# Kernel tuning notes

Measured on AMD Instinct MI355X. Metric: run time of the kernel, lower is better.

The kernel has to match this reference:

```python
import jax, jax.numpy as jnp
import numpy as np

B, T, D = 16, 4096, 1024
UNITS = 1024


def setup_inputs() -> dict:
    key = jax.random.key(0)
    ks = jax.random.split(key, 8)
    s_in = 1.0 / np.sqrt(D)
    s_u = 1.0 / np.sqrt(UNITS)
    return {
        "hidden_state": jax.random.normal(ks[0], (B, D), jnp.float32),
        "encoder_output": jax.random.normal(ks[1], (B, T, D), jnp.float32),
        "W1": jax.random.normal(ks[2], (D, UNITS), jnp.float32) * s_in,
        "b1": jnp.zeros((UNITS,), jnp.float32),
        "W2": jax.random.normal(ks[3], (D, UNITS), jnp.float32) * s_in,
        "b2": jnp.zeros((UNITS,), jnp.float32),
        "V": jax.random.normal(ks[4], (UNITS, 1), jnp.float32) * s_u,
        "bv": jnp.zeros((1,), jnp.float32),
    }


def reference(hidden_state, encoder_output, W1, b1, W2, b2, V, bv):
    # Bahdanau additive attention: score = V(tanh(W1(h) + W2(enc)))
    h_proj = hidden_state @ W1 + b1                      # [B, U]
    e_proj = jnp.einsum("btd,du->btu", encoder_output, W2) + b2  # [B, T, U]
    feat = jnp.tanh(h_proj[:, None, :] + e_proj)          # [B, T, U]
    score = feat @ V + bv                                 # [B, T, 1]
    attention_weights = jax.nn.softmax(score, axis=1)     # [B, T, 1]
    context_vector = jnp.sum(attention_weights * encoder_output, axis=1)  # [B, D]
    return context_vector, attention_weights
```

## Files before the change

kernel.cpp:

```cpp
#include <hip/hip_runtime.h>
#include <hip/hip_bf16.h>
#include <math.h>

#define B_ 16
#define T_ 4096
#define D_ 1024
#define U_ 1024
#define M_ (B_*T_)

typedef __attribute__((ext_vector_type(8))) short short8;
typedef __attribute__((ext_vector_type(4))) short short4v;
typedef __attribute__((ext_vector_type(4))) float float4v;

static __device__ __forceinline__ short f2bf(float f) {
    unsigned u = __builtin_bit_cast(unsigned, f);
    u += 0x7FFFu + ((u >> 16) & 1u);
    return (short)(u >> 16);
}
static __device__ __forceinline__ float bf2f(short s) {
    unsigned u = ((unsigned)(unsigned short)s) << 16;
    return __builtin_bit_cast(float, u);
}
static __device__ __forceinline__ float fast_tanh(float x) {
    float c = fminf(fmaxf(2.f * x, -30.f), 30.f);
    float t = __expf(c);
    return __fdividef(t - 1.f, t + 1.f);
}

#define GLLDS(GP, LP) __builtin_amdgcn_global_load_lds( \
    (const __attribute__((address_space(1))) void*)(GP), \
    (__attribute__((address_space(3))) void*)(LP), 16, 0, 0)

__global__ void hb_kernel(const float* __restrict__ h, const float* __restrict__ W1,
                          const float* __restrict__ b1, const float* __restrict__ b2,
                          float* __restrict__ hbp) {
    int x = blockIdx.x;
    int kc = x >> 6;
    int gid = (x & 63) * 256 + threadIdx.x;
    int b = gid >> 10, u = gid & 1023;
    const float* hr = h + b * D_ + kc * 256;
    const float* w = W1 + (size_t)(kc * 256) * U_ + u;
    float s0 = 0.f, s1 = 0.f, s2 = 0.f, s3 = 0.f;
    for (int k = 0; k < 256; k += 4) {
        s0 += hr[k+0] * w[(size_t)(k+0) * U_];
        s1 += hr[k+1] * w[(size_t)(k+1) * U_];
        s2 += hr[k+2] * w[(size_t)(k+2) * U_];
        s3 += hr[k+3] * w[(size_t)(k+3) * U_];
    }
    float s = ((s0 + s1) + (s2 + s3));
    if (kc == 0) s += b1[u] + b2[u];
    hbp[kc * 16384 + gid] = s;
}

__global__ void convert_enc(const float* __restrict__ enc, short* __restrict__ encbf) {
    size_t g = (size_t)blockIdx.x * 256 + threadIdx.x;
    const float4v* p = (const float4v*)(enc + g * 16);
    float4v f0 = p[0], f1 = p[1], f2 = p[2], f3 = p[3];
    short8 a, b;
    a[0]=f2bf(f0[0]); a[1]=f2bf(f0[1]); a[2]=f2bf(f0[2]); a[3]=f2bf(f0[3]);
    a[4]=f2bf(f1[0]); a[5]=f2bf(f1[1]); a[6]=f2bf(f1[2]); a[7]=f2bf(f1[3]);
    b[0]=f2bf(f2[0]); b[1]=f2bf(f2[1]); b[2]=f2bf(f2[2]); b[3]=f2bf(f2[3]);
    b[4]=f2bf(f3[0]); b[5]=f2bf(f3[1]); b[6]=f2bf(f3[2]); b[7]=f2bf(f3[3]);
    short8* q = (short8*)(encbf + g * 16);
    q[0] = a; q[1] = b;
}

__global__ void convert_w2t(const float* __restrict__ W2, short* __restrict__ W2T) {
    __shared__ short t[64][65];
    int k0 = (blockIdx.x >> 4) * 64, u0 = (blockIdx.x & 15) * 64;
    int tx = threadIdx.x & 63, ty = threadIdx.x >> 6;
    #pragma unroll
    for (int r = 0; r < 16; ++r) {
        int kk = ty * 16 + r;
        t[kk][tx] = f2bf(W2[(size_t)(k0 + kk) * U_ + u0 + tx]);
    }
    __syncthreads();
    #pragma unroll
    for (int r = 0; r < 16; ++r) {
        int uu = ty * 16 + r;
        W2T[(size_t)(u0 + uu) * D_ + k0 + tx] = t[tx][uu];
    }
}

__global__ __launch_bounds__(512, 2) void gemm_score_8ph(
    const short* __restrict__ Abf,
    const short* __restrict__ W2T,
    const float* __restrict__ hbp,
    const float* __restrict__ V,
    float* __restrict__ scorepart)
{
    __shared__ __align__(16) short lds[65536];

    const int tid = threadIdx.x;
    const int g = blockIdx.x;
    const int c = g & 7, q = g >> 3;
    const int ntile = q & 3;
    const int mtile = (q >> 2) * 8 + c;
    const int row0 = mtile * 256, n0 = ntile * 256;
    const int bidx = row0 >> 12;

    const int lane = tid & 63;
    const int wv = tid >> 6;
    const int wm = wv >> 2, wn = wv & 3;
    const int lm = lane & 15, quad = lane >> 4;

    const int srow = tid >> 3;
    const int lslot = (tid & 7) ^ (srow & 7);
    const short* aS = Abf + (size_t)(row0 + srow) * D_ + lslot * 8;
    const short* bS = W2T + (size_t)(n0  + srow) * D_ + lslot * 8;
    short* aD = lds + tid * 8;
    short* bD = lds + 32768 + tid * 8;

#define STG_A(kt, h, bf) do { \
    GLLDS(aS + (size_t)((h) * 128) * D_ + (kt) * 64,      aD + (bf) * 16384 + (h) * 8192); \
    GLLDS(aS + (size_t)((h) * 128 + 64) * D_ + (kt) * 64, aD + (bf) * 16384 + (h) * 8192 + 4096); \
} while (0)
#define STG_B(kt, h, bf) do { \
    GLLDS(bS + (size_t)((h) * 128) * D_ + (kt) * 64,      bD + (bf) * 16384 + (h) * 8192); \
    GLLDS(bS + (size_t)((h) * 128 + 64) * D_ + (kt) * 64, bD + (bf) * 16384 + (h) * 8192 + 4096); \
} while (0)
#define LDS_RD(off) (*(const short8*)(lds + (off)))
#define MFMA(a, b, c) __builtin_amdgcn_mfma_f32_16x16x32_bf16((a), (b), (c), 0, 0, 0)

    const int aB0 = (wm * 128 + lm) * 64 + (quad ^ (lm & 7)) * 8;
    const int aB1 = aB0 ^ 32;
    const int bB0 = 32768 + (wn * 64 + lm) * 64 + (quad ^ (lm & 7)) * 8;
    const int bB1 = bB0 ^ 32;

    float4v acc[8][4] = {};
    short8 Af[4][2], Bf[4][2];

    STG_A(0, 0, 0); STG_A(0, 1, 0); STG_B(0, 0, 0); STG_B(0, 1, 0);
    STG_B(1, 0, 1); STG_A(1, 0, 1); STG_B(1, 1, 1);
    asm volatile("s_waitcnt vmcnt(6)" ::: "memory");
    __builtin_amdgcn_s_barrier();
    __builtin_amdgcn_sched_barrier(0);

    for (int t = 0; t < 16; ++t) {
        const int buf = t & 1;
        const int ab = buf * 16384;
        #pragma unroll
        for (int mi = 0; mi < 4; ++mi) {
            Af[mi][0] = LDS_RD(ab + aB0 + mi * 1024);
            Af[mi][1] = LDS_RD(ab + aB1 + mi * 1024);
        }
        #pragma unroll
        for (int ni = 0; ni < 2; ++ni) {
            Bf[ni][0] = LDS_RD(ab + bB0 + ni * 1024);
            Bf[ni][1] = LDS_RD(ab + bB1 + ni * 1024);
        }
        if (t < 15) STG_A(t + 1, 1, (t + 1) & 1);
        __builtin_amdgcn_s_barrier();
        __builtin_amdgcn_s_setprio(1);
        #pragma unroll
        for (int mi = 0; mi < 4; ++mi)
            #pragma unroll
            for (int ni = 0; ni < 2; ++ni) {
                acc[mi][ni] = MFMA(Af[mi][0], Bf[ni][0], acc[mi][ni]);
                acc[mi][ni] = MFMA(Af[mi][1], Bf[ni][1], acc[mi][ni]);
            }
        __builtin_amdgcn_s_setprio(0);
        __builtin_amdgcn_s_barrier();
        #pragma unroll
        for (int ni = 0; ni < 2; ++ni) {
            Bf[2 + ni][0] = LDS_RD(ab + bB0 + (2 + ni) * 1024);
            Bf[2 + ni][1] = LDS_RD(ab + bB1 + (2 + ni) * 1024);
        }
        __builtin_amdgcn_s_barrier();
        __builtin_amdgcn_s_setprio(1);
        #pragma unroll
        for (int mi = 0; mi < 4; ++mi)
            #pragma unroll
            for (int ni = 0; ni < 2; ++ni) {
                acc[mi][2 + ni] = MFMA(Af[mi][0], Bf[2 + ni][0], acc[mi][2 + ni]);
                acc[mi][2 + ni] = MFMA(Af[mi][1], Bf[2 + ni][1], acc[mi][2 + ni]);
            }
        __builtin_amdgcn_s_setprio(0);
        __builtin_amdgcn_s_barrier();
        #pragma unroll
        for (int mi = 0; mi < 4; ++mi) {
            Af[mi][0] = LDS_RD(ab + aB0 + 4096 + mi * 1024);
            Af[mi][1] = LDS_RD(ab + aB1 + 4096 + mi * 1024);
        }
        if (t < 14) STG_B(t + 2, 0, buf);
        __builtin_amdgcn_s_barrier();
        __builtin_amdgcn_s_setprio(1);
        #pragma unroll
        for (int mi = 0; mi < 4; ++mi)
            #pragma unroll
            for (int ni = 0; ni < 2; ++ni) {
                acc[4 + mi][ni] = MFMA(Af[mi][0], Bf[ni][0], acc[4 + mi][ni]);
                acc[4 + mi][ni] = MFMA(Af[mi][1], Bf[ni][1], acc[4 + mi][ni]);
            }
        __builtin_amdgcn_s_setprio(0);
        __builtin_amdgcn_s_barrier();
        if (t < 14) { STG_A(t + 2, 0, buf); STG_B(t + 2, 1, buf); }
        __builtin_amdgcn_s_barrier();
        __builtin_amdgcn_s_setprio(1);
        #pragma unroll
        for (int mi = 0; mi < 4; ++mi)
            #pragma unroll
            for (int ni = 0; ni < 2; ++ni) {
                acc[4 + mi][2 + ni] = MFMA(Af[mi][0], Bf[2 + ni][0], acc[4 + mi][2 + ni]);
                acc[4 + mi][2 + ni] = MFMA(Af[mi][1], Bf[2 + ni][1], acc[4 + mi][2 + ni]);
            }
        __builtin_amdgcn_s_setprio(0);
        if (t < 14)      { asm volatile("s_waitcnt vmcnt(6)" ::: "memory"); }
        else if (t == 14){ asm volatile("s_waitcnt vmcnt(0)" ::: "memory"); }
        __builtin_amdgcn_s_barrier();
        __builtin_amdgcn_sched_barrier(0);
    }

    float* sbuf = (float*)lds;
    float hbv[4], Vv[4];
    #pragma unroll
    for (int ni = 0; ni < 4; ++ni) {
        int U = n0 + wn * 64 + ni * 16 + lm;
        int o = bidx * U_ + U;
        hbv[ni] = hbp[o] + hbp[16384 + o] + hbp[32768 + o] + hbp[49152 + o];
        Vv[ni]  = V[U];
    }
    #pragma unroll
    for (int mi = 0; mi < 8; ++mi) {
        #pragma unroll
        for (int r = 0; r < 4; ++r) {
            float s = 0.f;
            #pragma unroll
            for (int ni = 0; ni < 4; ++ni)
                s += fast_tanh(acc[mi][ni][r] + hbv[ni]) * Vv[ni];
            #pragma unroll
            for (int off = 1; off < 16; off <<= 1)
                s += __shfl_xor(s, off, 64);
            if (lm == 0)
                sbuf[wn * 256 + wm * 128 + mi * 16 + quad * 4 + r] = s;
        }
    }
    __syncthreads();
    if (tid < 256)
        scorepart[(size_t)ntile * M_ + row0 + tid] =
            sbuf[tid] + sbuf[256 + tid] + sbuf[512 + tid] + sbuf[768 + tid];
}

__global__ __launch_bounds__(1024) void softmax_kernel(
        const float* __restrict__ scorepart,
        const float* __restrict__ bv,
        float* __restrict__ out_attn) {
    __shared__ float sm[T_];
    __shared__ float redm[16];
    __shared__ float reds[16];
    int b = blockIdx.x, tid = threadIdx.x;
    int wv = tid >> 6;
    float bvv = bv[0];
    float lmax = -1e30f;
    #pragma unroll
    for (int i = 0; i < 4; ++i) {
        int t = tid + i * 1024;
        float s = bvv;
        #pragma unroll
        for (int p = 0; p < 4; ++p) s += scorepart[(size_t)p * M_ + b * T_ + t];
        sm[t] = s;
        lmax = fmaxf(lmax, s);
    }
    #pragma unroll
    for (int off = 1; off < 64; off <<= 1) lmax = fmaxf(lmax, __shfl_xor(lmax, off, 64));
    if ((tid & 63) == 0) redm[wv] = lmax;
    __syncthreads();
    float m = redm[0];
    #pragma unroll
    for (int j = 1; j < 16; ++j) m = fmaxf(m, redm[j]);
    float lsum = 0.f;
    #pragma unroll
    for (int i = 0; i < 4; ++i) {
        int t = tid + i * 1024;
        float e = __expf(sm[t] - m);
        sm[t] = e;
        lsum += e;
    }
    #pragma unroll
    for (int off = 1; off < 64; off <<= 1) lsum += __shfl_xor(lsum, off, 64);
    if ((tid & 63) == 0) reds[wv] = lsum;
    __syncthreads();
    float tot = 0.f;
    #pragma unroll
    for (int j = 0; j < 16; ++j) tot += reds[j];
    float rinv = 1.f / tot;
    #pragma unroll
    for (int i = 0; i < 4; ++i) {
        int t = tid + i * 1024;
        out_attn[b * T_ + t] = sm[t] * rinv;
    }
}

__global__ void ctx_part_bf(const short* __restrict__ encbf,
                            const float* __restrict__ attn,
                            float* __restrict__ part) {
    __shared__ float wsm[128];
    int x = blockIdx.x;
    int b = x & 15, tc = x >> 4;
    int tid = threadIdx.x;
    if (tid < 128) wsm[tid] = attn[b * T_ + tc * 128 + tid];
    __syncthreads();
    const short* e0 = encbf + (size_t)(b * T_ + tc * 128) * D_ + tid * 4;
    float4v acc = {};
    for (int t = 0; t < 128; ++t) {
        short4v v = *(const short4v*)(e0 + (size_t)t * D_);
        float w = wsm[t];
        acc[0] += w * bf2f(v[0]);
        acc[1] += w * bf2f(v[1]);
        acc[2] += w * bf2f(v[2]);
        acc[3] += w * bf2f(v[3]);
    }
    *(float4v*)(part + (size_t)x * 1024 + tid * 4) = acc;
}

__global__ void ctx_reduce_kernel(const float* __restrict__ part, float* __restrict__ ctx) {
    int gid = blockIdx.x * 256 + threadIdx.x;
    int b = gid >> 10, d = gid & 1023;
    float s = 0.f;
    #pragma unroll
    for (int tc = 0; tc < 32; ++tc) s += part[(size_t)(tc * 16 + b) * 1024 + d];
    ctx[gid] = s;
}

extern "C" void kernel_launch(void* const* d_in, const int* in_sizes, int n_in,
                              void* d_out, int out_size, void* d_ws, size_t ws_size,
                              hipStream_t stream) {
    const float* h   = (const float*)d_in[0];
    const float* enc = (const float*)d_in[1];
    const float* W1  = (const float*)d_in[2];
    const float* b1  = (const float*)d_in[3];
    const float* W2  = (const float*)d_in[4];
    const float* b2  = (const float*)d_in[5];
    const float* V   = (const float*)d_in[6];
    const float* bv  = (const float*)d_in[7];
    float* out = (float*)d_out;
    float* ws  = (float*)d_ws;

    float* hbp       = ws;
    float* scorepart = ws + 65536;
    float* ctxpart   = scorepart;
    short* W2T   = (short*)(ws + 65536 + 524288);
    short* encbf = (short*)((char*)W2T + (size_t)U_ * D_ * 2);

    hb_kernel<<<256, 256, 0, stream>>>(h, W1, b1, b2, hbp);
    convert_enc<<<16384, 256, 0, stream>>>(enc, encbf);
    convert_w2t<<<256, 256, 0, stream>>>(W2, W2T);
    gemm_score_8ph<<<1024, 512, 0, stream>>>(encbf, W2T, hbp, V, scorepart);
    softmax_kernel<<<16, 1024, 0, stream>>>(scorepart, bv, out + 16384);
    ctx_part_bf<<<512, 256, 0, stream>>>(encbf, out + 16384, ctxpart);
    ctx_reduce_kernel<<<64, 256, 0, stream>>>(ctxpart, out);
}
```

Before: 575.7 us.

## Fuse prep kernels into one launch and merge softmax into context pass

Merges the three preprocessing kernels (hidden projection, encoder bf16 conversion, W2 transpose) into one launch that branches on block index. Folds the softmax into the context-partial kernel: each of the 512 blocks recomputes the full-row max and sum for its batch and writes only its own 128-slice of attention weights. The context loop now uses 8-wide bf16 loads and two row-parity halves combined through LDS. This removes two launches and the serial 16-block softmax, at the cost of redundant softmax reductions (32x per batch row) and relocating ctxpart into the W2T region.

```diff
diff --git a/kernel.cpp b/kernel.cpp
--- a/kernel.cpp
+++ b/kernel.cpp
@@ -31,54 +31,55 @@
     (const __attribute__((address_space(1))) void*)(GP), \
     (__attribute__((address_space(3))) void*)(LP), 16, 0, 0)
 
-__global__ void hb_kernel(const float* __restrict__ h, const float* __restrict__ W1,
-                          const float* __restrict__ b1, const float* __restrict__ b2,
-                          float* __restrict__ hbp) {
-    int x = blockIdx.x;
-    int kc = x >> 6;
-    int gid = (x & 63) * 256 + threadIdx.x;
-    int b = gid >> 10, u = gid & 1023;
-    const float* hr = h + b * D_ + kc * 256;
-    const float* w = W1 + (size_t)(kc * 256) * U_ + u;
-    float s0 = 0.f, s1 = 0.f, s2 = 0.f, s3 = 0.f;
-    for (int k = 0; k < 256; k += 4) {
-        s0 += hr[k+0] * w[(size_t)(k+0) * U_];
-        s1 += hr[k+1] * w[(size_t)(k+1) * U_];
-        s2 += hr[k+2] * w[(size_t)(k+2) * U_];
-        s3 += hr[k+3] * w[(size_t)(k+3) * U_];
-    }
-    float s = ((s0 + s1) + (s2 + s3));
-    if (kc == 0) s += b1[u] + b2[u];
-    hbp[kc * 16384 + gid] = s;
-}
-
-__global__ void convert_enc(const float* __restrict__ enc, short* __restrict__ encbf) {
-    size_t g = (size_t)blockIdx.x * 256 + threadIdx.x;
-    const float4v* p = (const float4v*)(enc + g * 16);
-    float4v f0 = p[0], f1 = p[1], f2 = p[2], f3 = p[3];
-    short8 a, b;
-    a[0]=f2bf(f0[0]); a[1]=f2bf(f0[1]); a[2]=f2bf(f0[2]); a[3]=f2bf(f0[3]);
-    a[4]=f2bf(f1[0]); a[5]=f2bf(f1[1]); a[6]=f2bf(f1[2]); a[7]=f2bf(f1[3]);
-    b[0]=f2bf(f2[0]); b[1]=f2bf(f2[1]); b[2]=f2bf(f2[2]); b[3]=f2bf(f2[3]);
-    b[4]=f2bf(f3[0]); b[5]=f2bf(f3[1]); b[6]=f2bf(f3[2]); b[7]=f2bf(f3[3]);
-    short8* q = (short8*)(encbf + g * 16);
-    q[0] = a; q[1] = b;
-}
-
-__global__ void convert_w2t(const float* __restrict__ W2, short* __restrict__ W2T) {
-    __shared__ short t[64][65];
-    int k0 = (blockIdx.x >> 4) * 64, u0 = (blockIdx.x & 15) * 64;
-    int tx = threadIdx.x & 63, ty = threadIdx.x >> 6;
-    #pragma unroll
-    for (int r = 0; r < 16; ++r) {
-        int kk = ty * 16 + r;
-        t[kk][tx] = f2bf(W2[(size_t)(k0 + kk) * U_ + u0 + tx]);
-    }
-    __syncthreads();
-    #pragma unroll
-    for (int r = 0; r < 16; ++r) {
-        int uu = ty * 16 + r;
-        W2T[(size_t)(u0 + uu) * D_ + k0 + tx] = t[tx][uu];
+__global__ void prep_fused(const float* __restrict__ h, const float* __restrict__ W1,
+                           const float* __restrict__ b1, const float* __restrict__ b2,
+                           const float* __restrict__ W2, const float* __restrict__ enc,
+                           float* __restrict__ hbp, short* __restrict__ W2T,
+                           short* __restrict__ encbf) {
+    int bx = blockIdx.x;
+    if (bx >= 512) {
+        size_t g = (size_t)(bx - 512) * 256 + threadIdx.x;
+        const float4v* p = (const float4v*)(enc + g * 16);
+        float4v f0 = p[0], f1 = p[1], f2 = p[2], f3 = p[3];
+        short8 a, b;
+        a[0]=f2bf(f0[0]); a[1]=f2bf(f0[1]); a[2]=f2bf(f0[2]); a[3]=f2bf(f0[3]);
+        a[4]=f2bf(f1[0]); a[5]=f2bf(f1[1]); a[6]=f2bf(f1[2]); a[7]=f2bf(f1[3]);
+        b[0]=f2bf(f2[0]); b[1]=f2bf(f2[1]); b[2]=f2bf(f2[2]); b[3]=f2bf(f2[3]);
+        b[4]=f2bf(f3[0]); b[5]=f2bf(f3[1]); b[6]=f2bf(f3[2]); b[7]=f2bf(f3[3]);
+        short8* q = (short8*)(encbf + g * 16);
+        q[0] = a; q[1] = b;
+    } else if (bx < 256) {
+        int kc = bx >> 6;
+        int gid = (bx & 63) * 256 + threadIdx.x;
+        int b = gid >> 10, u = gid & 1023;
+        const float* hr = h + b * D_ + kc * 256;
+        const float* w = W1 + (size_t)(kc * 256) * U_ + u;
+        float s0 = 0.f, s1 = 0.f, s2 = 0.f, s3 = 0.f;
+        for (int k = 0; k < 256; k += 4) {
+            s0 += hr[k+0] * w[(size_t)(k+0) * U_];
+            s1 += hr[k+1] * w[(size_t)(k+1) * U_];
+            s2 += hr[k+2] * w[(size_t)(k+2) * U_];
+            s3 += hr[k+3] * w[(size_t)(k+3) * U_];
+        }
+        float s = ((s0 + s1) + (s2 + s3));
+        if (kc == 0) s += b1[u] + b2[u];
+        hbp[kc * 16384 + gid] = s;
+    } else {
+        __shared__ short t[64][65];
+        int x = bx - 256;
+        int k0 = (x >> 4) * 64, u0 = (x & 15) * 64;
+        int tx = threadIdx.x & 63, ty = threadIdx.x >> 6;
+        #pragma unroll
+        for (int r = 0; r < 16; ++r) {
+            int kk = ty * 16 + r;
+            t[kk][tx] = f2bf(W2[(size_t)(k0 + kk) * U_ + u0 + tx]);
+        }
+        __syncthreads();
+        #pragma unroll
+        for (int r = 0; r < 16; ++r) {
+            int uu = ty * 16 + r;
+            W2T[(size_t)(u0 + uu) * D_ + k0 + tx] = t[tx][uu];
+        }
     }
 }
 
@@ -241,76 +242,77 @@
             sbuf[tid] + sbuf[256 + tid] + sbuf[512 + tid] + sbuf[768 + tid];
 }
 
-__global__ __launch_bounds__(1024) void softmax_kernel(
+__global__ __launch_bounds__(256) void ctx_softmax(
         const float* __restrict__ scorepart,
         const float* __restrict__ bv,
-        float* __restrict__ out_attn) {
+        const short* __restrict__ encbf,
+        float* __restrict__ out_attn,
+        float* __restrict__ part)
+{
     __shared__ float sm[T_];
-    __shared__ float redm[16];
-    __shared__ float reds[16];
-    int b = blockIdx.x, tid = threadIdx.x;
-    int wv = tid >> 6;
-    float bvv = bv[0];
+    __shared__ float wsm[128];
+    __shared__ float lacc[1024];
+    __shared__ float red[8];
+    const int x = blockIdx.x, tid = threadIdx.x;
+    const int b = x & 15, tc = x >> 4;
+    const int wvi = tid >> 6;
+    const float bv0 = bv[0];
     float lmax = -1e30f;
     #pragma unroll
-    for (int i = 0; i < 4; ++i) {
-        int t = tid + i * 1024;
-        float s = bvv;
-        #pragma unroll
-        for (int p = 0; p < 4; ++p) s += scorepart[(size_t)p * M_ + b * T_ + t];
+    for (int i = 0; i < 16; ++i) {
+        int t = tid + i * 256;
+        const float* sp = scorepart + (size_t)b * T_ + t;
+        float s = bv0 + sp[0] + sp[M_] + sp[2 * (size_t)M_] + sp[3 * (size_t)M_];
         sm[t] = s;
         lmax = fmaxf(lmax, s);
     }
     #pragma unroll
     for (int off = 1; off < 64; off <<= 1) lmax = fmaxf(lmax, __shfl_xor(lmax, off, 64));
-    if ((tid & 63) == 0) redm[wv] = lmax;
-    __syncthreads();
-    float m = redm[0];
-    #pragma unroll
-    for (int j = 1; j < 16; ++j) m = fmaxf(m, redm[j]);
+    if ((tid & 63) == 0) red[wvi] = lmax;
+    __syncthreads();
+    const float m = fmaxf(fmaxf(red[0], red[1]), fmaxf(red[2], red[3]));
     float lsum = 0.f;
     #pragma unroll
-    for (int i = 0; i < 4; ++i) {
-        int t = tid + i * 1024;
-        float e = __expf(sm[t] - m);
-        sm[t] = e;
-        lsum += e;
-    }
+    for (int i = 0; i < 16; ++i) lsum += __expf(sm[tid + i * 256] - m);
     #pragma unroll
     for (int off = 1; off < 64; off <<= 1) lsum += __shfl_xor(lsum, off, 64);
-    if ((tid & 63) == 0) reds[wv] = lsum;
-    __syncthreads();
-    float tot = 0.f;
-    #pragma unroll
-    for (int j = 0; j < 16; ++j) tot += reds[j];
-    float rinv = 1.f / tot;
-    #pragma unroll
-    for (int i = 0; i < 4; ++i) {
-        int t = tid + i * 1024;
-        out_attn[b * T_ + t] = sm[t] * rinv;
-    }
-}
-
-__global__ void ctx_part_bf(const short* __restrict__ encbf,
-                            const float* __restrict__ attn,
-                            float* __restrict__ part) {
-    __shared__ float wsm[128];
-    int x = blockIdx.x;
-    int b = x & 15, tc = x >> 4;
-    int tid = threadIdx.x;
-    if (tid < 128) wsm[tid] = attn[b * T_ + tc * 128 + tid];
-    __syncthreads();
-    const short* e0 = encbf + (size_t)(b * T_ + tc * 128) * D_ + tid * 4;
-    float4v acc = {};
-    for (int t = 0; t < 128; ++t) {
-        short4v v = *(const short4v*)(e0 + (size_t)t * D_);
-        float w = wsm[t];
-        acc[0] += w * bf2f(v[0]);
-        acc[1] += w * bf2f(v[1]);
-        acc[2] += w * bf2f(v[2]);
-        acc[3] += w * bf2f(v[3]);
-    }
-    *(float4v*)(part + (size_t)x * 1024 + tid * 4) = acc;
+    if ((tid & 63) == 0) red[4 + wvi] = lsum;
+    __syncthreads();
+    const float tot = (red[4] + red[5]) + (red[6] + red[7]);
+    const float rinv = 1.f / tot;
+    if ((tid >> 7) == (tc & 1)) {
+        int j = tid & 127;
+        int t = tc * 128 + j;
+        float w = __expf(sm[t] - m) * rinv;
+        wsm[j] = w;
+        out_attn[b * T_ + t] = w;
+    }
+    __syncthreads();
+    const int par = tid >> 7;
+    const int d0 = (tid & 127) * 8;
+    const short* e0 = encbf + (size_t)(b * T_ + tc * 128 + par) * D_ + d0;
+    float4v a0 = {}, a1 = {};
+    #pragma unroll 4
+    for (int it = 0; it < 64; ++it) {
+        short8 v = *(const short8*)(e0 + (size_t)it * 2 * D_);
+        float w = wsm[it * 2 + par];
+        a0[0] += w * bf2f(v[0]); a0[1] += w * bf2f(v[1]);
+        a0[2] += w * bf2f(v[2]); a0[3] += w * bf2f(v[3]);
+        a1[0] += w * bf2f(v[4]); a1[1] += w * bf2f(v[5]);
+        a1[2] += w * bf2f(v[6]); a1[3] += w * bf2f(v[7]);
+    }
+    if (par) {
+        *(float4v*)(lacc + (tid & 127) * 8)     = a0;
+        *(float4v*)(lacc + (tid & 127) * 8 + 4) = a1;
+    }
+    __syncthreads();
+    if (!par) {
+        const float* l = lacc + tid * 8;
+        a0[0] += l[0]; a0[1] += l[1]; a0[2] += l[2]; a0[3] += l[3];
+        a1[0] += l[4]; a1[1] += l[5]; a1[2] += l[6]; a1[3] += l[7];
+        float4v* pp = (float4v*)(part + (size_t)x * 1024 + tid * 8);
+        pp[0] = a0; pp[1] = a1;
+    }
 }
 
 __global__ void ctx_reduce_kernel(const float* __restrict__ part, float* __restrict__ ctx) {
@@ -338,15 +340,12 @@
 
     float* hbp       = ws;
     float* scorepart = ws + 65536;
-    float* ctxpart   = scorepart;
     short* W2T   = (short*)(ws + 65536 + 524288);
+    float* ctxpart   = (float*)W2T;
     short* encbf = (short*)((char*)W2T + (size_t)U_ * D_ * 2);
 
-    hb_kernel<<<256, 256, 0, stream>>>(h, W1, b1, b2, hbp);
-    convert_enc<<<16384, 256, 0, stream>>>(enc, encbf);
-    convert_w2t<<<256, 256, 0, stream>>>(W2, W2T);
+    prep_fused<<<16896, 256, 0, stream>>>(h, W1, b1, b2, W2, enc, hbp, W2T, encbf);
     gemm_score_8ph<<<1024, 512, 0, stream>>>(encbf, W2T, hbp, V, scorepart);
-    softmax_kernel<<<16, 1024, 0, stream>>>(scorepart, bv, out + 16384);
-    ctx_part_bf<<<512, 256, 0, stream>>>(encbf, out + 16384, ctxpart);
+    ctx_softmax<<<512, 256, 0, stream>>>(scorepart, bv, encbf, out + 16384, ctxpart);
     ctx_reduce_kernel<<<64, 256, 0, stream>>>(ctxpart, out);
 }
```

Result: faster. 559.3 us (-2.8%).
